# Kernel optimization log

Measured on AMD Instinct MI355X. Metric: run time of the kernel, lower is better.

Reference implementation:

```python
import jax, jax.numpy as jnp
import numpy as np

N = 100000
E = 1600000
F_IN = 512
H1, C1 = 8, 8      # layer-1: 8 heads, 8 dims each (concat -> 64)
H2, C2 = 1, 16     # layer-2: 1 head, num_classes=16
SLOPE = 0.2        # GATConv leaky_relu negative slope


def setup_inputs() -> dict:
    key = jax.random.key(0)
    ks = jax.random.split(key, 10)
    x = jax.random.normal(ks[0], (N, F_IN), dtype=jnp.float32)
    edge_index = jax.random.randint(ks[1], (2, E), 0, N, dtype=jnp.int32)
    s = 0.05
    W1 = jax.random.normal(ks[2], (F_IN, H1 * C1), dtype=jnp.float32) * s
    a1_src = jax.random.normal(ks[3], (H1, C1), dtype=jnp.float32) * s
    a1_dst = jax.random.normal(ks[4], (H1, C1), dtype=jnp.float32) * s
    b1 = jnp.zeros((H1 * C1,), dtype=jnp.float32)
    W2 = jax.random.normal(ks[5], (H1 * C1, H2 * C2), dtype=jnp.float32) * s
    a2_src = jax.random.normal(ks[6], (H2, C2), dtype=jnp.float32) * s
    a2_dst = jax.random.normal(ks[7], (H2, C2), dtype=jnp.float32) * s
    b2 = jnp.zeros((H2 * C2,), dtype=jnp.float32)
    return {"x": x, "edge_index": edge_index, "W1": W1, "a1_src": a1_src,
            "a1_dst": a1_dst, "b1": b1, "W2": W2, "a2_src": a2_src,
            "a2_dst": a2_dst, "b2": b2}


def _gat_conv(h, src, dst, W, a_src, a_dst, b, heads, ch):
    n = h.shape[0]
    hp = (h @ W).reshape(n, heads, ch)                      # [N,H,C]
    al_s = jnp.einsum('nhc,hc->nh', hp, a_src)              # [N,H]
    al_d = jnp.einsum('nhc,hc->nh', hp, a_dst)              # [N,H]
    e = jax.nn.leaky_relu(al_s[src] + al_d[dst], SLOPE)     # [E,H]
    # segment softmax over edges sharing a destination (self-loops guarantee >=1 edge/node)
    emax = jax.lax.stop_gradient(jax.ops.segment_max(e, dst, num_segments=n))
    ee = jnp.exp(e - emax[dst])
    denom = jax.ops.segment_sum(ee, dst, num_segments=n)
    alpha = ee / denom[dst]                                 # [E,H]
    msg = hp[src] * alpha[:, :, None]                       # [E,H,C]
    out = jax.ops.segment_sum(msg, dst, num_segments=n)     # [N,H,C]
    return out.reshape(n, heads * ch) + b


def reference(x, edge_index, W1, a1_src, a1_dst, b1, W2, a2_src, a2_dst, b2):
    n = x.shape[0]
    loops = jnp.arange(n, dtype=edge_index.dtype)           # add_self_loops=True
    src = jnp.concatenate([edge_index[0], loops])
    dst = jnp.concatenate([edge_index[1], loops])
    h = jax.nn.elu(_gat_conv(x, src, dst, W1, a1_src, a1_dst, b1, H1, C1))
    h = _gat_conv(h, src, dst, W2, a2_src, a2_dst, b2, H2, C2)
    return jax.nn.log_softmax(h, axis=1)
```

## Files before the change

### kernel.cpp

```cpp
#include <hip/hip_runtime.h>
#include <hip/hip_bf16.h>

#define N_NODES 100000
#define F_IN    512
#define H1      8
#define C1      8
#define D1      64
#define C2      16
#define SLOPE   0.2f
#define CAP     48
#define PSHIFT  9
#define PPART   196
#define CAPP    9216
#define CHUNK   4096

typedef __bf16 bf16_t;
typedef bf16_t bf16x8 __attribute__((ext_vector_type(8)));
typedef float  f32x4  __attribute__((ext_vector_type(4)));

__global__ __launch_bounds__(256) void wcvt_kernel(
    const float* __restrict__ W, bf16_t* __restrict__ Bt)
{
    int i = blockIdx.x * 256 + threadIdx.x;
    if (i >= 64 * 512) return;
    int nn = i >> 9, k = i & 511;
    Bt[i] = (bf16_t)W[k * 64 + nn];
}

__global__ __launch_bounds__(256) void part_kernel(
    const int* __restrict__ ei, int* __restrict__ pcnt, int2* __restrict__ pfifo,
    int E, int total)
{
    __shared__ int hist[PPART];
    __shared__ int lofs[PPART];
    __shared__ int gbase[PPART];
    __shared__ int cursor[PPART];
    __shared__ int sdata[256];
    __shared__ int2 fifo[CHUNK];

    const int t = threadIdx.x;
    const int chunk0 = (int)blockIdx.x * CHUNK;

    for (int i = t; i < PPART; i += 256) hist[i] = 0;
    __syncthreads();

    int srcs[16], dsts[16];
    const int e0 = chunk0 + t * 16;
    if (e0 + 16 <= E) {
#pragma unroll
        for (int q = 0; q < 4; ++q) {
            int4 s = *(const int4*)(ei + e0 + q * 4);
            int4 d = *(const int4*)(ei + E + e0 + q * 4);
            srcs[q*4+0]=s.x; srcs[q*4+1]=s.y; srcs[q*4+2]=s.z; srcs[q*4+3]=s.w;
            dsts[q*4+0]=d.x; dsts[q*4+1]=d.y; dsts[q*4+2]=d.z; dsts[q*4+3]=d.w;
        }
    } else {
#pragma unroll
        for (int j = 0; j < 16; ++j) {
            int e = e0 + j;
            if (e < E)          { srcs[j] = ei[e]; dsts[j] = ei[E + e]; }
            else if (e < total) { srcs[j] = dsts[j] = e - E; }
            else                { srcs[j] = -1;    dsts[j] = -1; }
        }
    }
#pragma unroll
    for (int j = 0; j < 16; ++j)
        if (dsts[j] >= 0) atomicAdd(&hist[dsts[j] >> PSHIFT], 1);
    __syncthreads();

    int hv = (t < PPART) ? hist[t] : 0;
    sdata[t] = hv;
    __syncthreads();
    for (int off = 1; off < 256; off <<= 1) {
        int x = (t >= off) ? sdata[t - off] : 0;
        __syncthreads();
        sdata[t] += x;
        __syncthreads();
    }
    if (t < PPART) {
        int lo = sdata[t] - hv;
        lofs[t]   = lo;
        cursor[t] = lo;
        gbase[t]  = hv ? atomicAdd(&pcnt[t], hv) : 0;
    }
    __syncthreads();

#pragma unroll
    for (int j = 0; j < 16; ++j) {
        if (dsts[j] >= 0) {
            int p = dsts[j] >> PSHIFT;
            int slot = atomicAdd(&cursor[p], 1);
            fifo[slot] = make_int2(srcs[j], dsts[j]);
        }
    }
    __syncthreads();

    const int w = t >> 6, lane = t & 63;
    for (int p = w; p < PPART; p += 4) {
        int len = hist[p];
        int lo  = lofs[p];
        int gb  = gbase[p];
        int2* dstp = pfifo + (size_t)p * CAPP;
        for (int j = lane; j < len; j += 64) {
            int g = gb + j;
            if (g < CAPP) dstp[g] = fifo[lo + j];
        }
    }
}

__global__ __launch_bounds__(256) void place_kernel(
    const int2* __restrict__ pfifo, const int* __restrict__ pcnt,
    int* __restrict__ buckets, int* __restrict__ cnt, int n)
{
    __shared__ int lcnt[1 << PSHIFT];
    const int p = blockIdx.x;
    const int dbase = p << PSHIFT;
    const int nd = min(1 << PSHIFT, n - dbase);
    const int t = threadIdx.x;
    for (int i = t; i < nd; i += 256) lcnt[i] = 0;
    __syncthreads();

    int len = pcnt[p]; if (len > CAPP) len = CAPP;
    const int2* f = pfifo + (size_t)p * CAPP;

    int i = t;
    for (; i + 768 < len; i += 1024) {
        int2 e0 = f[i], e1 = f[i + 256], e2 = f[i + 512], e3 = f[i + 768];
        int s0 = atomicAdd(&lcnt[e0.y - dbase], 1);
        int s1 = atomicAdd(&lcnt[e1.y - dbase], 1);
        int s2 = atomicAdd(&lcnt[e2.y - dbase], 1);
        int s3 = atomicAdd(&lcnt[e3.y - dbase], 1);
        if (s0 < CAP) buckets[(size_t)e0.y * CAP + s0] = e0.x;
        if (s1 < CAP) buckets[(size_t)e1.y * CAP + s1] = e1.x;
        if (s2 < CAP) buckets[(size_t)e2.y * CAP + s2] = e2.x;
        if (s3 < CAP) buckets[(size_t)e3.y * CAP + s3] = e3.x;
    }
    for (; i < len; i += 256) {
        int2 e = f[i];
        int s = atomicAdd(&lcnt[e.y - dbase], 1);
        if (s < CAP) buckets[(size_t)e.y * CAP + s] = e.x;
    }
    __syncthreads();
    for (int i2 = t; i2 < nd; i2 += 256) cnt[dbase + i2] = min(lcnt[i2], CAP);
}

__global__ __launch_bounds__(512, 4) void gemm1_kernel(
    const float* __restrict__ X, const bf16_t* __restrict__ Bt,
    const float* __restrict__ a1s, const float* __restrict__ a1d,
    bf16_t* __restrict__ HPb, float* __restrict__ als1, float* __restrict__ ald1,
    int n)
{
    __shared__ __align__(16) bf16_t Bsm[8 * 4 * 64 * 8];

    const int t = threadIdx.x;
    const int rowbase = (int)blockIdx.x * 128;
    const int w = t >> 6;
    const int lane = t & 63;

    const int rloc = lane & 15;
    const int koff = (lane >> 4) * 8;

    int grow = rowbase + w * 16 + rloc;
    int growc = (grow < n) ? grow : (n - 1);
    const float* arow = X + (size_t)growc * F_IN + koff;

    f32x4 acc[4];
#pragma unroll
    for (int nt = 0; nt < 4; ++nt) acc[nt] = (f32x4){0.f, 0.f, 0.f, 0.f};

#pragma unroll
    for (int half = 0; half < 2; ++half) {
        for (int i = t; i < 2048; i += 512) {
            int l9 = i & 63;
            int nt = (i >> 6) & 3;
            int ks = i >> 8;
            int row = nt * 16 + (l9 & 15);
            int col = (half * 8 + ks) * 32 + (l9 >> 4) * 8;
            *(bf16x8*)(Bsm + (size_t)i * 8) =
                *(const bf16x8*)(Bt + (size_t)row * F_IN + col);
        }
        __syncthreads();

#pragma unroll 4
        for (int ks = 0; ks < 8; ++ks) {
            int kg = (half * 8 + ks) * 32;
            float4 xa0 = *(const float4*)(arow + kg);
            float4 xa1 = *(const float4*)(arow + kg + 4);
            bf16x8 af;
            af[0]=(bf16_t)xa0.x; af[1]=(bf16_t)xa0.y; af[2]=(bf16_t)xa0.z; af[3]=(bf16_t)xa0.w;
            af[4]=(bf16_t)xa1.x; af[5]=(bf16_t)xa1.y; af[6]=(bf16_t)xa1.z; af[7]=(bf16_t)xa1.w;
#pragma unroll
            for (int nt = 0; nt < 4; ++nt) {
                bf16x8 b = *(const bf16x8*)(Bsm + ((ks * 4 + nt) * 64 + lane) * 8);
                acc[nt] = __builtin_amdgcn_mfma_f32_16x16x32_bf16(af, b, acc[nt], 0, 0, 0);
            }
        }
        __syncthreads();
    }

    const int colg = lane & 15;
    const int quad = lane >> 4;
    const int b    = colg >> 3;
    float cs[4], cd[4];
#pragma unroll
    for (int nt = 0; nt < 4; ++nt) {
        cs[nt] = a1s[nt * 16 + colg];
        cd[nt] = a1d[nt * 16 + colg];
    }

#pragma unroll
    for (int i = 0; i < 4; ++i) {
        int r = rowbase + w * 16 + quad * 4 + i;
        bool ok = r < n;
        if (ok) {
            bf16_t* hr = HPb + (size_t)r * D1;
            hr[colg]      = (bf16_t)acc[0][i];
            hr[16 + colg] = (bf16_t)acc[1][i];
            hr[32 + colg] = (bf16_t)acc[2][i];
            hr[48 + colg] = (bf16_t)acc[3][i];
        }
#pragma unroll
        for (int nt = 0; nt < 4; ++nt) {
            float ps = acc[nt][i] * cs[nt];
            float pd = acc[nt][i] * cd[nt];
            ps += __shfl_xor(ps, 1, 64);  pd += __shfl_xor(pd, 1, 64);
            ps += __shfl_xor(ps, 2, 64);  pd += __shfl_xor(pd, 2, 64);
            ps += __shfl_xor(ps, 4, 64);  pd += __shfl_xor(pd, 4, 64);
            if (ok && (colg & 7) == 0) {
                als1[(size_t)r * 8 + 2 * nt + b] = ps;
                ald1[(size_t)r * 8 + 2 * nt + b] = pd;
            }
        }
    }
}

__global__ __launch_bounds__(256) void agg1_kernel(
    const bf16_t* __restrict__ hp1,
    const float* __restrict__ als, const float* __restrict__ ald,
    const int* __restrict__ cnt, const int* __restrict__ buckets,
    const float* __restrict__ b1,
    float* __restrict__ h1, int n)
{
    int node = blockIdx.x * 4 + (threadIdx.x >> 6);
    if (node >= n) return;
    int lane = threadIdx.x & 63;
    int h = lane >> 3;

    int m = cnt[node]; if (m > CAP) m = CAP;
    const int* bp = buckets + (size_t)node * CAP;
    float ad = ald[node * 8 + h];
    float den = 0.f, acc = 0.f;

    int i = 0;
    for (; i + 8 <= m; i += 8) {
        int s0 = bp[i + 0], s1 = bp[i + 1], s2 = bp[i + 2], s3 = bp[i + 3];
        int s4 = bp[i + 4], s5 = bp[i + 5], s6 = bp[i + 6], s7 = bp[i + 7];
        float a0 = als[s0 * 8 + h], a1 = als[s1 * 8 + h];
        float a2 = als[s2 * 8 + h], a3 = als[s3 * 8 + h];
        float a4 = als[s4 * 8 + h], a5 = als[s5 * 8 + h];
        float a6 = als[s6 * 8 + h], a7 = als[s7 * 8 + h];
        float v0 = (float)hp1[(size_t)s0 * D1 + lane];
        float v1 = (float)hp1[(size_t)s1 * D1 + lane];
        float v2 = (float)hp1[(size_t)s2 * D1 + lane];
        float v3 = (float)hp1[(size_t)s3 * D1 + lane];
        float v4 = (float)hp1[(size_t)s4 * D1 + lane];
        float v5 = (float)hp1[(size_t)s5 * D1 + lane];
        float v6 = (float)hp1[(size_t)s6 * D1 + lane];
        float v7 = (float)hp1[(size_t)s7 * D1 + lane];
        float e0 = a0 + ad; e0 = (e0 > 0.f) ? e0 : SLOPE * e0;
        float e1 = a1 + ad; e1 = (e1 > 0.f) ? e1 : SLOPE * e1;
        float e2 = a2 + ad; e2 = (e2 > 0.f) ? e2 : SLOPE * e2;
        float e3 = a3 + ad; e3 = (e3 > 0.f) ? e3 : SLOPE * e3;
        float e4 = a4 + ad; e4 = (e4 > 0.f) ? e4 : SLOPE * e4;
        float e5 = a5 + ad; e5 = (e5 > 0.f) ? e5 : SLOPE * e5;
        float e6 = a6 + ad; e6 = (e6 > 0.f) ? e6 : SLOPE * e6;
        float e7 = a7 + ad; e7 = (e7 > 0.f) ? e7 : SLOPE * e7;
        float w0 = __expf(e0), w1 = __expf(e1), w2 = __expf(e2), w3 = __expf(e3);
        float w4 = __expf(e4), w5 = __expf(e5), w6 = __expf(e6), w7 = __expf(e7);
        den += ((w0 + w1) + (w2 + w3)) + ((w4 + w5) + (w6 + w7));
        acc = fmaf(w0, v0, acc);
        acc = fmaf(w1, v1, acc);
        acc = fmaf(w2, v2, acc);
        acc = fmaf(w3, v3, acc);
        acc = fmaf(w4, v4, acc);
        acc = fmaf(w5, v5, acc);
        acc = fmaf(w6, v6, acc);
        acc = fmaf(w7, v7, acc);
    }
    for (; i < m; ++i) {
        int s = bp[i];
        float e = als[s * 8 + h] + ad;
        e = (e > 0.f) ? e : SLOPE * e;
        float ee = __expf(e);
        den += ee;
        acc = fmaf(ee, (float)hp1[(size_t)s * D1 + lane], acc);
    }
    float v = acc / den + b1[lane];
    v = (v > 0.f) ? v : (__expf(v) - 1.f);
    h1[(size_t)node * D1 + lane] = v;
}

__global__ __launch_bounds__(256) void gemm2_kernel(
    const float* __restrict__ H, const float* __restrict__ W2,
    const float* __restrict__ a2s, const float* __restrict__ a2d,
    bf16_t* __restrict__ HP2b, float* __restrict__ als2, float* __restrict__ ald2,
    int n)
{
    __shared__ float Ws[64 * 16];
    int t = threadIdx.x;
    for (int i = t; i < 1024; i += 256) Ws[i] = W2[i];
    __syncthreads();
    int idx = blockIdx.x * 256 + t;
    int node = idx >> 4, c = idx & 15;
    if (node >= n) return;
    const float* hr = H + (size_t)node * D1;
    float acc = 0.f;
#pragma unroll 8
    for (int k = 0; k < 64; ++k) acc = fmaf(hr[k], Ws[k * 16 + c], acc);
    HP2b[idx] = (bf16_t)acc;

    float rs = acc * a2s[c];
    float rd = acc * a2d[c];
    rs += __shfl_xor(rs, 8, 16);  rd += __shfl_xor(rd, 8, 16);
    rs += __shfl_xor(rs, 4, 16);  rd += __shfl_xor(rd, 4, 16);
    rs += __shfl_xor(rs, 2, 16);  rd += __shfl_xor(rd, 2, 16);
    rs += __shfl_xor(rs, 1, 16);  rd += __shfl_xor(rd, 1, 16);
    if (c == 0) { als2[node] = rs; ald2[node] = rd; }
}

__global__ __launch_bounds__(256) void agg2_kernel(
    const bf16_t* __restrict__ hp2,
    const float* __restrict__ als, const float* __restrict__ ald,
    const int* __restrict__ cnt, const int* __restrict__ buckets,
    const float* __restrict__ b2,
    float* __restrict__ out, int n)
{
    int node = blockIdx.x * 16 + (threadIdx.x >> 4);
    if (node >= n) return;
    int c = threadIdx.x & 15;

    int m0c = cnt[node]; if (m0c > CAP) m0c = CAP;
    const int* bp = buckets + (size_t)node * CAP;
    float ad = ald[node];
    float den = 0.f, acc = 0.f;

    int i = 0;
    for (; i + 8 <= m0c; i += 8) {
        int s0 = bp[i + 0], s1 = bp[i + 1], s2 = bp[i + 2], s3 = bp[i + 3];
        int s4 = bp[i + 4], s5 = bp[i + 5], s6 = bp[i + 6], s7 = bp[i + 7];
        float a0 = als[s0], a1 = als[s1], a2 = als[s2], a3 = als[s3];
        float a4 = als[s4], a5 = als[s5], a6 = als[s6], a7 = als[s7];
        float v0 = (float)hp2[(size_t)s0 * 16 + c];
        float v1 = (float)hp2[(size_t)s1 * 16 + c];
        float v2 = (float)hp2[(size_t)s2 * 16 + c];
        float v3 = (float)hp2[(size_t)s3 * 16 + c];
        float v4 = (float)hp2[(size_t)s4 * 16 + c];
        float v5 = (float)hp2[(size_t)s5 * 16 + c];
        float v6 = (float)hp2[(size_t)s6 * 16 + c];
        float v7 = (float)hp2[(size_t)s7 * 16 + c];
        float e0 = a0 + ad; e0 = (e0 > 0.f) ? e0 : SLOPE * e0;
        float e1 = a1 + ad; e1 = (e1 > 0.f) ? e1 : SLOPE * e1;
        float e2 = a2 + ad; e2 = (e2 > 0.f) ? e2 : SLOPE * e2;
        float e3 = a3 + ad; e3 = (e3 > 0.f) ? e3 : SLOPE * e3;
        float e4 = a4 + ad; e4 = (e4 > 0.f) ? e4 : SLOPE * e4;
        float e5 = a5 + ad; e5 = (e5 > 0.f) ? e5 : SLOPE * e5;
        float e6 = a6 + ad; e6 = (e6 > 0.f) ? e6 : SLOPE * e6;
        float e7 = a7 + ad; e7 = (e7 > 0.f) ? e7 : SLOPE * e7;
        float w0 = __expf(e0), w1 = __expf(e1), w2 = __expf(e2), w3 = __expf(e3);
        float w4 = __expf(e4), w5 = __expf(e5), w6 = __expf(e6), w7 = __expf(e7);
        den += ((w0 + w1) + (w2 + w3)) + ((w4 + w5) + (w6 + w7));
        acc = fmaf(w0, v0, acc);
        acc = fmaf(w1, v1, acc);
        acc = fmaf(w2, v2, acc);
        acc = fmaf(w3, v3, acc);
        acc = fmaf(w4, v4, acc);
        acc = fmaf(w5, v5, acc);
        acc = fmaf(w6, v6, acc);
        acc = fmaf(w7, v7, acc);
    }
    for (; i < m0c; ++i) {
        int s = bp[i];
        float e = als[s] + ad;
        e = (e > 0.f) ? e : SLOPE * e;
        float ee = __expf(e);
        den += ee;
        acc = fmaf(ee, (float)hp2[(size_t)s * 16 + c], acc);
    }
    float v = acc / den + b2[c];

    float m = v;
    m = fmaxf(m, __shfl_xor(m, 8, 16));
    m = fmaxf(m, __shfl_xor(m, 4, 16));
    m = fmaxf(m, __shfl_xor(m, 2, 16));
    m = fmaxf(m, __shfl_xor(m, 1, 16));
    float ex = __expf(v - m);
    float sum = ex;
    sum += __shfl_xor(sum, 8, 16);
    sum += __shfl_xor(sum, 4, 16);
    sum += __shfl_xor(sum, 2, 16);
    sum += __shfl_xor(sum, 1, 16);
    out[(size_t)node * 16 + c] = v - m - __logf(sum);
}

extern "C" void kernel_launch(void* const* d_in, const int* in_sizes, int n_in,
                              void* d_out, int out_size, void* d_ws, size_t ws_size,
                              hipStream_t stream)
{
    const float* x      = (const float*)d_in[0];
    const int*   ei     = (const int*)  d_in[1];
    const float* W1     = (const float*)d_in[2];
    const float* a1_src = (const float*)d_in[3];
    const float* a1_dst = (const float*)d_in[4];
    const float* b1     = (const float*)d_in[5];
    const float* W2     = (const float*)d_in[6];
    const float* a2_src = (const float*)d_in[7];
    const float* a2_dst = (const float*)d_in[8];
    const float* b2     = (const float*)d_in[9];
    float* out = (float*)d_out;

    const int N = in_sizes[0] / F_IN;
    const int E = in_sizes[1] / 2;
    const int TOT = E + N;

    char* base = (char*)d_ws;
    size_t off = 0;
    auto carve = [&](size_t bytes) -> char* {
        char* p = base + off;
        off += (bytes + 255) & ~(size_t)255;
        return p;
    };
    bf16_t* hp1b    = (bf16_t*)carve((size_t)N * D1 * 2);
    float*  h1      = (float*) carve((size_t)N * D1 * 4);
    bf16_t* hp2b    = (bf16_t*)carve((size_t)N * 16 * 2);
    float*  als1    = (float*) carve((size_t)N * 8 * 4);
    float*  ald1    = (float*) carve((size_t)N * 8 * 4);
    float*  als2    = (float*) carve((size_t)N * 4);
    float*  ald2    = (float*) carve((size_t)N * 4);
    int*    cnt     = (int*)   carve((size_t)N * 4);
    int*    pcnt    = (int*)   carve((size_t)PPART * 4);
    int*    buckets = (int*)   carve((size_t)N * CAP * 4);
    bf16_t* W1b     = (bf16_t*)carve((size_t)64 * 512 * 2);
    int2*  pfifo   = (int2*)h1;

    const int Gp = (TOT + CHUNK - 1) / CHUNK;

    hipMemsetAsync(pcnt, 0, (size_t)PPART * 4, stream);

    wcvt_kernel<<<128, 256, 0, stream>>>(W1, W1b);
    part_kernel<<<Gp, 256, 0, stream>>>(ei, pcnt, pfifo, E, TOT);
    place_kernel<<<PPART, 256, 0, stream>>>(pfifo, pcnt, buckets, cnt, N);

    gemm1_kernel<<<(N + 127) / 128, 512, 0, stream>>>(x, W1b, a1_src, a1_dst,
                                                      hp1b, als1, ald1, N);

    agg1_kernel<<<(N + 3) / 4, 256, 0, stream>>>(hp1b, als1, ald1, cnt, buckets, b1, h1, N);

    gemm2_kernel<<<(N * 16 + 255) / 256, 256, 0, stream>>>(h1, W2, a2_src, a2_dst, hp2b, als2, ald2, N);

    agg2_kernel<<<(N + 15) / 16, 256, 0, stream>>>(hp2b, als2, ald2, cnt, buckets, b2, out, N);
}
```

Measured before the change: 507.4 us.

## Fuse layer-2 projection into agg1 and fold weight conversion into partition kernel

The layer-2 linear projection and attention logits are now computed inside the layer-1 aggregation kernel, using wave shuffles over the ELU output and a padded shared-memory copy of W2. This removes the fp32 h1 round trip through global memory and one kernel launch. The W1 bf16 transpose is folded into the partition kernel with a grid-stride loop, dropping another launch. The place kernel now uses 512 threads per block. Each agg1 block adds a W2 load into shared memory plus a barrier, and the per-node shuffle reduction adds some compute.

After: 507.9 us. Within noise of the previous version (+0.1%).

```diff
diff --git a/kernel.cpp b/kernel.cpp
--- a/kernel.cpp
+++ b/kernel.cpp
@@ -18,16 +18,8 @@
 typedef bf16_t bf16x8 __attribute__((ext_vector_type(8)));
 typedef float  f32x4  __attribute__((ext_vector_type(4)));
 
-__global__ __launch_bounds__(256) void wcvt_kernel(
-    const float* __restrict__ W, bf16_t* __restrict__ Bt)
-{
-    int i = blockIdx.x * 256 + threadIdx.x;
-    if (i >= 64 * 512) return;
-    int nn = i >> 9, k = i & 511;
-    Bt[i] = (bf16_t)W[k * 64 + nn];
-}
-
 __global__ __launch_bounds__(256) void part_kernel(
+    const float* __restrict__ W1, bf16_t* __restrict__ W1b,
     const int* __restrict__ ei, int* __restrict__ pcnt, int2* __restrict__ pfifo,
     int E, int total)
 {
@@ -40,6 +32,11 @@
 
     const int t = threadIdx.x;
     const int chunk0 = (int)blockIdx.x * CHUNK;
+
+    for (int i = (int)blockIdx.x * 256 + t; i < 64 * 512; i += (int)gridDim.x * 256) {
+        int nn = i >> 9, k = i & 511;
+        W1b[i] = (bf16_t)W1[k * 64 + nn];
+    }
 
     for (int i = t; i < PPART; i += 256) hist[i] = 0;
     __syncthreads();
@@ -108,7 +105,7 @@
     }
 }
 
-__global__ __launch_bounds__(256) void place_kernel(
+__global__ __launch_bounds__(512) void place_kernel(
     const int2* __restrict__ pfifo, const int* __restrict__ pcnt,
     int* __restrict__ buckets, int* __restrict__ cnt, int n)
 {
@@ -117,15 +114,15 @@
     const int dbase = p << PSHIFT;
     const int nd = min(1 << PSHIFT, n - dbase);
     const int t = threadIdx.x;
-    for (int i = t; i < nd; i += 256) lcnt[i] = 0;
+    for (int i = t; i < nd; i += 512) lcnt[i] = 0;
     __syncthreads();
 
     int len = pcnt[p]; if (len > CAPP) len = CAPP;
     const int2* f = pfifo + (size_t)p * CAPP;
 
     int i = t;
-    for (; i + 768 < len; i += 1024) {
-        int2 e0 = f[i], e1 = f[i + 256], e2 = f[i + 512], e3 = f[i + 768];
+    for (; i + 1536 < len; i += 2048) {
+        int2 e0 = f[i], e1 = f[i + 512], e2 = f[i + 1024], e3 = f[i + 1536];
         int s0 = atomicAdd(&lcnt[e0.y - dbase], 1);
         int s1 = atomicAdd(&lcnt[e1.y - dbase], 1);
         int s2 = atomicAdd(&lcnt[e2.y - dbase], 1);
@@ -135,13 +132,13 @@
         if (s2 < CAP) buckets[(size_t)e2.y * CAP + s2] = e2.x;
         if (s3 < CAP) buckets[(size_t)e3.y * CAP + s3] = e3.x;
     }
-    for (; i < len; i += 256) {
+    for (; i < len; i += 512) {
         int2 e = f[i];
         int s = atomicAdd(&lcnt[e.y - dbase], 1);
         if (s < CAP) buckets[(size_t)e.y * CAP + s] = e.x;
     }
     __syncthreads();
-    for (int i2 = t; i2 < nd; i2 += 256) cnt[dbase + i2] = min(lcnt[i2], CAP);
+    for (int i2 = t; i2 < nd; i2 += 512) cnt[dbase + i2] = min(lcnt[i2], CAP);
 }
 
 __global__ __launch_bounds__(512, 4) void gemm1_kernel(
@@ -239,11 +236,20 @@
     const float* __restrict__ als, const float* __restrict__ ald,
     const int* __restrict__ cnt, const int* __restrict__ buckets,
     const float* __restrict__ b1,
-    float* __restrict__ h1, int n)
-{
-    int node = blockIdx.x * 4 + (threadIdx.x >> 6);
+    const float* __restrict__ W2,
+    const float* __restrict__ a2s, const float* __restrict__ a2d,
+    bf16_t* __restrict__ HP2b, float* __restrict__ als2, float* __restrict__ ald2,
+    int n)
+{
+    __shared__ float Wsm[64 * 17];
+    const int t = threadIdx.x;
+    for (int i = t; i < 1024; i += 256)
+        Wsm[(i >> 4) * 17 + (i & 15)] = W2[i];
+    __syncthreads();
+
+    int node = blockIdx.x * 4 + (t >> 6);
     if (node >= n) return;
-    int lane = threadIdx.x & 63;
+    int lane = t & 63;
     int h = lane >> 3;
 
     int m = cnt[node]; if (m > CAP) m = CAP;
@@ -297,35 +303,25 @@
     }
     float v = acc / den + b1[lane];
     v = (v > 0.f) ? v : (__expf(v) - 1.f);
-    h1[(size_t)node * D1 + lane] = v;
-}
-
-__global__ __launch_bounds__(256) void gemm2_kernel(
-    const float* __restrict__ H, const float* __restrict__ W2,
-    const float* __restrict__ a2s, const float* __restrict__ a2d,
-    bf16_t* __restrict__ HP2b, float* __restrict__ als2, float* __restrict__ ald2,
-    int n)
-{
-    __shared__ float Ws[64 * 16];
-    int t = threadIdx.x;
-    for (int i = t; i < 1024; i += 256) Ws[i] = W2[i];
-    __syncthreads();
-    int idx = blockIdx.x * 256 + t;
-    int node = idx >> 4, c = idx & 15;
-    if (node >= n) return;
-    const float* hr = H + (size_t)node * D1;
-    float acc = 0.f;
-#pragma unroll 8
-    for (int k = 0; k < 64; ++k) acc = fmaf(hr[k], Ws[k * 16 + c], acc);
-    HP2b[idx] = (bf16_t)acc;
-
-    float rs = acc * a2s[c];
-    float rd = acc * a2d[c];
-    rs += __shfl_xor(rs, 8, 16);  rd += __shfl_xor(rd, 8, 16);
-    rs += __shfl_xor(rs, 4, 16);  rd += __shfl_xor(rd, 4, 16);
-    rs += __shfl_xor(rs, 2, 16);  rd += __shfl_xor(rd, 2, 16);
-    rs += __shfl_xor(rs, 1, 16);  rd += __shfl_xor(rd, 1, 16);
-    if (c == 0) { als2[node] = rs; ald2[node] = rd; }
+
+    const int g = lane >> 4, c = lane & 15;
+    float o = 0.f;
+#pragma unroll
+    for (int kk = 0; kk < 16; ++kk) {
+        float hk = __shfl(v, g * 16 + kk, 64);
+        o = fmaf(hk, Wsm[(g * 16 + kk) * 17 + c], o);
+    }
+    o += __shfl_xor(o, 16, 64);
+    o += __shfl_xor(o, 32, 64);
+    if (g == 0) HP2b[(size_t)node * 16 + c] = (bf16_t)o;
+
+    float rs = o * a2s[c];
+    float rd = o * a2d[c];
+    rs += __shfl_xor(rs, 1, 64);  rd += __shfl_xor(rd, 1, 64);
+    rs += __shfl_xor(rs, 2, 64);  rd += __shfl_xor(rd, 2, 64);
+    rs += __shfl_xor(rs, 4, 64);  rd += __shfl_xor(rd, 4, 64);
+    rs += __shfl_xor(rs, 8, 64);  rd += __shfl_xor(rd, 8, 64);
+    if (lane == 0) { als2[node] = rs; ald2[node] = rd; }
 }
 
 __global__ __launch_bounds__(256) void agg2_kernel(
@@ -446,16 +442,15 @@
 
     hipMemsetAsync(pcnt, 0, (size_t)PPART * 4, stream);
 
-    wcvt_kernel<<<128, 256, 0, stream>>>(W1, W1b);
-    part_kernel<<<Gp, 256, 0, stream>>>(ei, pcnt, pfifo, E, TOT);
-    place_kernel<<<PPART, 256, 0, stream>>>(pfifo, pcnt, buckets, cnt, N);
+    part_kernel<<<Gp, 256, 0, stream>>>(W1, W1b, ei, pcnt, pfifo, E, TOT);
+    place_kernel<<<PPART, 512, 0, stream>>>(pfifo, pcnt, buckets, cnt, N);
 
     gemm1_kernel<<<(N + 127) / 128, 512, 0, stream>>>(x, W1b, a1_src, a1_dst,
                                                       hp1b, als1, ald1, N);
 
-    agg1_kernel<<<(N + 3) / 4, 256, 0, stream>>>(hp1b, als1, ald1, cnt, buckets, b1, h1, N);
-
-    gemm2_kernel<<<(N * 16 + 255) / 256, 256, 0, stream>>>(h1, W2, a2_src, a2_dst, hp2b, als2, ald2, N);
+    agg1_kernel<<<(N + 3) / 4, 256, 0, stream>>>(hp1b, als1, ald1, cnt, buckets,
+                                                 b1, W2, a2_src, a2_dst,
+                                                 hp2b, als2, ald2, N);
 
     agg2_kernel<<<(N + 15) / 16, 256, 0, stream>>>(hp2b, als2, ald2, cnt, buckets, b2, out, N);
 }
```
